# Performance work log

Measured on AMD Instinct MI355X. Metric: run time of the kernel, lower is better.

The kernel has to match this reference:

```python
import jax, jax.numpy as jnp
import numpy as np

B, X, C = 8192, 8, 512        # batch, map_num, img_dim==tex_dim
P, Y = 8, 1000                # n_prompts, cls_num
FAKE = 16                     # fake prompt width (hardcoded in module)
F = 2048                      # feat_dim
CLS = 1000                    # cls_num
IN_DIM = P * X * FAKE         # 1024
SF = 64.0


def setup_inputs() -> dict:
    key = jax.random.key(0)
    ks = jax.random.split(key, 8)
    s = 0.02
    return {
        "img_f": jax.random.normal(ks[0], (B, X, C), jnp.float32),
        "tex_f": jax.random.normal(ks[1], (P, Y, C), jnp.float32),
        "fake_cls": jax.random.normal(ks[2], (P, FAKE, C), jnp.float32),
        "fc_w": jax.random.normal(ks[3], (C, C), jnp.float32) * s,
        "fc_b": jnp.zeros((C,), jnp.float32),
        "bn1_g": jnp.ones((IN_DIM,), jnp.float32),
        "bn1_b": jnp.zeros((IN_DIM,), jnp.float32),
        "w1": jax.random.normal(ks[4], (F, IN_DIM), jnp.float32) * s,
        "b1": jnp.zeros((F,), jnp.float32),
        "bn2_g": jnp.ones((F,), jnp.float32),
        "bn2_b": jnp.zeros((F,), jnp.float32),
        "w2": jax.random.normal(ks[5], (CLS, F), jnp.float32) * s,
        "b2": jnp.zeros((CLS,), jnp.float32),
    }


def _bn(x, g, b, eps=1e-5):
    # BatchNorm1d in training mode: batch mean / biased batch var
    m = x.mean(axis=0)
    v = x.var(axis=0)
    return (x - m) * jax.lax.rsqrt(v + eps) * g + b


def reference(img_f, tex_f, fake_cls, fc_w, fc_b, bn1_g, bn1_b, w1, b1,
              bn2_g, bn2_b, w2, b2):
    # independent L2 norm over feature dim, scaled by x_sf=64
    img_n = img_f / (jnp.linalg.norm(img_f, axis=-1, keepdims=True) + 1e-6) * SF
    tex_n = tex_f / (jnp.linalg.norm(tex_f, axis=-1, keepdims=True) + 1e-6) * SF
    # prompt attention over the class axis
    tex_fc = jnp.einsum('pyc,dc->pyd', tex_n, fc_w) + fc_b          # fc(tex_f)
    attn = jax.nn.softmax(jnp.einsum('pxc,pyc->pxy', fake_cls, tex_fc), axis=-1)
    tex_a = jnp.einsum('pxy,pyc->pxc', attn, tex_n)                  # (P,16,C)
    # cross-modal relation: 'b x c, y d c -> b yxd' (icomp/tcomp are Identity)
    cp = jnp.einsum('bxc,pdc->bpxd', img_n, tex_a).reshape(img_n.shape[0], -1)
    # prt_fc: BN -> Linear -> ELU -> BN -> Linear
    h = jax.nn.elu(_bn(cp, bn1_g, bn1_b) @ w1.T + b1)
    return _bn(h, bn2_g, bn2_b) @ w2.T + b2
```

## Files before the change

kernel.cpp:

```cpp
#include <hip/hip_runtime.h>
#include <math.h>


typedef __attribute__((ext_vector_type(8))) short bf16x8;
typedef __attribute__((ext_vector_type(4))) float f32x4;

__device__ __forceinline__ float waveSum(float v) {
#pragma unroll
    for (int o = 32; o > 0; o >>= 1) v += __shfl_xor(v, o);
    return v;
}
__device__ __forceinline__ float waveMax(float v) {
#pragma unroll
    for (int o = 32; o > 0; o >>= 1) v = fmaxf(v, __shfl_xor(v, o));
    return v;
}
__device__ __forceinline__ unsigned short f2bf(float x) {
    union { float f; unsigned u; } v; v.f = x;
    unsigned r = v.u + 0x7FFFu + ((v.u >> 16) & 1u);
    return (unsigned short)(r >> 16);
}
__device__ __forceinline__ float bf2f(unsigned short h) {
    union { unsigned u; float f; } v; v.u = ((unsigned)h) << 16; return v.f;
}
__device__ __forceinline__ float bf2f_s(short h) { return bf2f((unsigned short)h); }
__device__ __forceinline__ void gload16(const void* g, const void* l) {
    __builtin_amdgcn_global_load_lds((const __attribute__((address_space(1))) void*)g,
                                     (__attribute__((address_space(3))) void*)l, 16, 0, 0);
}
__device__ __forceinline__ int xcd_swz(int d, int n) {
    int q = n >> 3;
    return (d & 7) * q + (d >> 3);
}
#define SBAR __builtin_amdgcn_sched_barrier(0)

__global__ __launch_bounds__(256) void k_prep(const float* __restrict__ tex_f,
                                              unsigned short* __restrict__ texn,
                                              const float* __restrict__ fake_cls,
                                              const float* __restrict__ fc_w,
                                              unsigned short* __restrict__ g_bf) {
    __shared__ float sred[4];
    __shared__ float fcls[512];
    int bid = blockIdx.x, t = threadIdx.x;
    if (bid < 8000) {
        const float* r = tex_f + (size_t)bid * 512;
        float2 v = *(const float2*)(r + t * 2);
        float ss = v.x * v.x + v.y * v.y;
        ss = waveSum(ss);
        if ((t & 63) == 0) sred[t >> 6] = ss;
        __syncthreads();
        float tot = sred[0] + sred[1] + sred[2] + sred[3];
        float sc = 64.f / (sqrtf(tot) + 1e-6f);
        unsigned u = (unsigned)f2bf(v.x * sc) | ((unsigned)f2bf(v.y * sc) << 16);
        *(unsigned*)(texn + (size_t)bid * 512 + t * 2) = u;
    } else {
        int row = bid - 8000;
        fcls[t]       = fake_cls[row * 512 + t];
        fcls[t + 256] = fake_cls[row * 512 + t + 256];
        __syncthreads();
        float a0 = 0.f, a1 = 0.f;
        for (int d = 0; d < 512; ++d) {
            float fv = fcls[d];
            a0 = fmaf(fv, fc_w[d * 512 + t], a0);
            a1 = fmaf(fv, fc_w[d * 512 + t + 256], a1);
        }
        g_bf[row * 512 + t]       = f2bf(a0);
        g_bf[row * 512 + t + 256] = f2bf(a1);
    }
}

__global__ __launch_bounds__(256) void k_wsum_sm(const float* __restrict__ logit,
                                                 const unsigned short* __restrict__ texn,
                                                 float* __restrict__ part) {
    int yt = blockIdx.x, p = blockIdx.y, t = threadIdx.x;
    int lane = t & 63, w = t >> 6;
    __shared__ float wl[16][63];
    __shared__ float ms[16], iss[16];
    const int y0 = yt * 63;
    const int ylen = min(63, 1000 - y0);
#pragma unroll
    for (int rr = 0; rr < 4; ++rr) {
        int x = w * 4 + rr;
        const float* lr = logit + ((size_t)p * 16 + x) * 1000;
        float m = -3.0e38f;
        for (int y = lane; y < 1000; y += 64) m = fmaxf(m, lr[y]);
        m = waveMax(m);
        float s = 0.f;
        for (int y = lane; y < 1000; y += 64) s += expf(lr[y] - m);
        s = waveSum(s);
        if (lane == 0) { ms[x] = m; iss[x] = 1.f / s; }
    }
    __syncthreads();
    for (int idx = t; idx < 16 * ylen; idx += 256) {
        int x = idx / ylen, y = idx % ylen;
        wl[x][y] = expf(logit[((size_t)p * 16 + x) * 1000 + y0 + y] - ms[x]) * iss[x];
    }
    __syncthreads();
    int c0 = t * 2;
    const unsigned short* tp = texn + ((size_t)p * 1000 + y0) * 512 + c0;
    float a0[16], a1[16];
#pragma unroll
    for (int x = 0; x < 16; ++x) { a0[x] = 0.f; a1[x] = 0.f; }
    for (int y = 0; y < ylen; ++y) {
        unsigned u = *(const unsigned*)(tp + (size_t)y * 512);
        float lo = bf2f((unsigned short)(u & 0xffff));
        float hi = bf2f((unsigned short)(u >> 16));
#pragma unroll
        for (int x = 0; x < 16; ++x) {
            float ww = wl[x][y];
            a0[x] = fmaf(ww, lo, a0[x]);
            a1[x] = fmaf(ww, hi, a1[x]);
        }
    }
#pragma unroll
    for (int x = 0; x < 16; ++x) {
        float* dst = part + ((size_t)((yt * 8 + p) * 16 + x)) * 512 + c0;
        dst[0] = a0[x];
        dst[1] = a1[x];
    }
}

__global__ __launch_bounds__(256) void k_texa_red(const float* __restrict__ part,
                                                  unsigned short* __restrict__ texa) {
    int row = blockIdx.x, t = threadIdx.x;
    int p = row >> 4, x = row & 15;
    int c = t * 2;
    float s0 = 0.f, s1 = 0.f;
#pragma unroll
    for (int yt = 0; yt < 16; ++yt) {
        const float* src = part + ((size_t)((yt * 8 + p) * 16 + x)) * 512 + c;
        s0 += src[0];
        s1 += src[1];
    }
    unsigned u = (unsigned)f2bf(s0) | ((unsigned)f2bf(s1) << 16);
    *(unsigned*)(texa + (size_t)row * 512 + c) = u;
}

__global__ __launch_bounds__(256) void k_colstat_v(const unsigned short* __restrict__ src,
                                                   float* __restrict__ ps,
                                                   float* __restrict__ pq) {
    const int cb = blockIdx.x, rb = blockIdx.y, t = threadIdx.x;
    const int tc = t & 15;
    const int tg = t >> 4;
    const unsigned short* base =
        src + (size_t)(rb * 128 + tg * 8) * 1024 + cb * 128 + tc * 8;
    float s[8], q[8];
#pragma unroll
    for (int j = 0; j < 8; ++j) { s[j] = 0.f; q[j] = 0.f; }
#pragma unroll
    for (int r = 0; r < 8; ++r) {
        bf16x8 v = *(const bf16x8*)(base + (size_t)r * 1024);
#pragma unroll
        for (int j = 0; j < 8; ++j) {
            float f = bf2f_s(v[j]);
            s[j] += f;
            q[j] = fmaf(f, f, q[j]);
        }
    }
    __shared__ float ls[16][128];
    __shared__ float lq[16][128];
#pragma unroll
    for (int j = 0; j < 8; ++j) { ls[tg][tc * 8 + j] = s[j]; lq[tg][tc * 8 + j] = q[j]; }
    __syncthreads();
    if (t < 128) {
        float S = 0.f, Q = 0.f;
#pragma unroll
        for (int g = 0; g < 16; ++g) { S += ls[g][t]; Q += lq[g][t]; }
        ps[(size_t)rb * 1024 + cb * 128 + t] = S;
        pq[(size_t)rb * 1024 + cb * 128 + t] = Q;
    }
}

template <bool PERM>
__global__ __launch_bounds__(256) void k_bnfin(const float* __restrict__ ps,
                                               const float* __restrict__ pq,
                                               const float* __restrict__ gam,
                                               const float* __restrict__ bet,
                                               float* __restrict__ a, float* __restrict__ c,
                                               int ncols) {
    int col = blockIdx.x * 256 + threadIdx.x;
    float S = 0.f, Q = 0.f;
    for (int i = 0; i < 64; ++i) {
        S += ps[(size_t)i * ncols + col];
        Q += pq[(size_t)i * ncols + col];
    }
    float mean = S * (1.f / 8192.f);
    float var = Q * (1.f / 8192.f) - mean * mean;
    int j = col;
    if (PERM) {
        int x = col >> 7, jj = col & 127, pp = jj >> 4, d = jj & 15;
        j = (pp << 7) + (x << 4) + d;
    }
    float av = gam[j] * rsqrtf(var + 1e-5f);
    a[col] = av;
    c[col] = bet[j] - mean * av;
}

template <bool PERM>
__global__ __launch_bounds__(256) void k_foldw_bf(const float* __restrict__ W,
                                                  const float* __restrict__ bin,
                                                  const float* __restrict__ a,
                                                  const float* __restrict__ c,
                                                  unsigned short* __restrict__ Wout,
                                                  float* __restrict__ bout,
                                                  int Kdim, int nvalid) {
    int f = blockIdx.x, t = threadIdx.x;
    unsigned short* wo = Wout + (size_t)f * Kdim;
    if (f >= nvalid) {
        for (int col = t; col < Kdim; col += 256) wo[col] = 0;
        if (t == 0) bout[f] = 0.f;
        return;
    }
    const float* wr = W + (size_t)f * Kdim;
    float partial = 0.f;
    for (int col = t; col < Kdim; col += 256) {
        int j = col;
        if (PERM) {
            int x = col >> 7, jj = col & 127, pp = jj >> 4, d = jj & 15;
            j = (pp << 7) + (x << 4) + d;
        }
        float wv = wr[j];
        wo[col] = f2bf(wv * a[col]);
        partial = fmaf(wv, c[col], partial);
    }
    partial = waveSum(partial);
    __shared__ float sred[4];
    if ((t & 63) == 0) sred[t >> 6] = partial;
    __syncthreads();
    if (t == 0) bout[f] = bin[f] + sred[0] + sred[1] + sred[2] + sred[3];
}

template <int EPI, bool A_F32>
__global__ __launch_bounds__(256) void gemm_mfma(const void* __restrict__ Av,
                                                 const unsigned short* __restrict__ Bv,
                                                 void* __restrict__ Cv, int K,
                                                 int ntn, int ldc, int nvalid,
                                                 int aZ, int bZ, int cZ) {
    __shared__ unsigned short Asl[128 * 64];
    __shared__ unsigned short Bsl[128 * 64];
    __shared__ float rowinv[128];
    const int tid = threadIdx.x;
    const int lane = tid & 63, wid = tid >> 6;
    const int wr = wid >> 1, wc = wid & 1;
    const int wg = xcd_swz(blockIdx.x, gridDim.x);
    const int m0 = (wg / ntn) * 128, n0 = (wg % ntn) * 128;
    const int z = blockIdx.y;

    const float* Af = (const float*)Av;
    const unsigned short* Ab = (const unsigned short*)Av + (size_t)z * aZ;
    const unsigned short* B = Bv + (size_t)z * bZ;

    f32x4 acc[4][4];
#pragma unroll
    for (int i = 0; i < 4; ++i)
#pragma unroll
        for (int j = 0; j < 4; ++j) acc[i][j] = {0.f, 0.f, 0.f, 0.f};

    const int swz = ((lane & 7) ^ (lane >> 3)) * 8;
    const int lrow = lane & 15, lkh = lane >> 4;
    float ssq[4] = {0.f, 0.f, 0.f, 0.f};

    for (int k0 = 0; k0 < K; k0 += 64) {
        if (A_F32) {
#pragma unroll
            for (int r = 0; r < 4; ++r) {
                int row = r * 32 + (tid >> 3);
                int kk = (tid & 7) * 8;
                const float* src = Af + (size_t)(m0 + row) * K + k0 + kk;
                float4 p0 = *(const float4*)src;
                float4 p1 = *(const float4*)(src + 4);
                ssq[r] += p0.x*p0.x + p0.y*p0.y + p0.z*p0.z + p0.w*p0.w
                        + p1.x*p1.x + p1.y*p1.y + p1.z*p1.z + p1.w*p1.w;
                bf16x8 v;
                v[0] = (short)f2bf(p0.x); v[1] = (short)f2bf(p0.y);
                v[2] = (short)f2bf(p0.z); v[3] = (short)f2bf(p0.w);
                v[4] = (short)f2bf(p1.x); v[5] = (short)f2bf(p1.y);
                v[6] = (short)f2bf(p1.z); v[7] = (short)f2bf(p1.w);
                *(bf16x8*)&Asl[row * 64 + (kk ^ ((row & 7) << 3))] = v;
            }
        } else {
#pragma unroll
            for (int r = 0; r < 4; ++r) {
                int row = r * 32 + wid * 8 + (lane >> 3);
                gload16(Ab + (size_t)(m0 + row) * K + k0 + swz,
                        Asl + r * 2048 + wid * 512);
            }
        }
#pragma unroll
        for (int r = 0; r < 4; ++r) {
            int row = r * 32 + wid * 8 + (lane >> 3);
            gload16(B + (size_t)(n0 + row) * K + k0 + swz,
                    Bsl + r * 2048 + wid * 512);
        }
        __syncthreads();
#pragma unroll
        for (int kk = 0; kk < 2; ++kk) {
            bf16x8 af[4], bfr[4];
#pragma unroll
            for (int m = 0; m < 4; ++m) {
                int row = wr * 64 + m * 16 + lrow;
                af[m] = *(const bf16x8*)&Asl[row * 64 + ((kk * 32 + lkh * 8) ^ ((row & 7) << 3))];
            }
#pragma unroll
            for (int n = 0; n < 4; ++n) {
                int row = wc * 64 + n * 16 + lrow;
                bfr[n] = *(const bf16x8*)&Bsl[row * 64 + ((kk * 32 + lkh * 8) ^ ((row & 7) << 3))];
            }
#pragma unroll
            for (int m = 0; m < 4; ++m)
#pragma unroll
                for (int n = 0; n < 4; ++n)
                    acc[m][n] = __builtin_amdgcn_mfma_f32_16x16x32_bf16(af[m], bfr[n], acc[m][n], 0, 0, 0);
        }
        __syncthreads();
    }

    if (A_F32) {
#pragma unroll
        for (int r = 0; r < 4; ++r) {
            float s = ssq[r];
            s += __shfl_xor(s, 1); s += __shfl_xor(s, 2); s += __shfl_xor(s, 4);
            if ((tid & 7) == 0) rowinv[r * 32 + (tid >> 3)] = 64.f / (sqrtf(s) + 1e-6f);
        }
        __syncthreads();
    }

    const int colbase = n0 + wc * 64 + lrow;
    if (EPI == 0) {
        unsigned short* C = (unsigned short*)Cv;
#pragma unroll
        for (int m = 0; m < 4; ++m) {
            int rloc = wr * 64 + m * 16 + lkh * 4;
#pragma unroll
            for (int r = 0; r < 4; ++r) {
                float riv = rowinv[rloc + r];
#pragma unroll
                for (int n = 0; n < 4; ++n)
                    C[(size_t)(m0 + rloc + r) * ldc + colbase + n * 16] = f2bf(acc[m][n][r] * riv);
            }
        }
    } else {
        float* C = (float*)Cv + (size_t)z * cZ;
#pragma unroll
        for (int m = 0; m < 4; ++m) {
            int row = m0 + wr * 64 + m * 16 + lkh * 4;
#pragma unroll
            for (int r = 0; r < 4; ++r) {
                if ((row + r) >= 16) continue;
#pragma unroll
                for (int n = 0; n < 4; ++n) {
                    int col = colbase + n * 16;
                    if (col < nvalid) C[(size_t)(row + r) * ldc + col] = acc[m][n][r];
                }
            }
        }
    }
}

template <int FM, int NH, int EPI>
__global__ __launch_bounds__(512, 2) void gemm256(const unsigned short* __restrict__ A,
                                                  const unsigned short* __restrict__ B,
                                                  void* __restrict__ Cv, int K,
                                                  int ntn, int ldc, int nvalid,
                                                  const float* __restrict__ bias,
                                                  float* __restrict__ ps,
                                                  float* __restrict__ pq) {
    constexpr int BM = FM * 32;
    constexpr int MH = BM / 128;
    constexpr int LA = 2 * (MH + NH);
    __shared__ unsigned short Asl[2][MH][128 * 64];
    __shared__ unsigned short Bsl[2][NH][128 * 64];
    const int tid = threadIdx.x;
    const int lane = tid & 63, wid = tid >> 6;
    const int wm = wid >> 2, wn = wid & 3;
    const int wg = xcd_swz(blockIdx.x, gridDim.x);
    const int m0 = (wg / ntn) * BM, n0 = (wg % ntn) * 256;
    const int lrow = lane & 15, lkh = lane >> 4;
    const int l7 = lane & 7;
    const int ksrc = ((lane & 7) ^ (lane >> 3)) * 8;
    const int mbase = wm * (BM / 2);
    const int mhalf = mbase >> 7;
    const int mloc0 = mbase & 127;
    const int nbase = wn * 64;
    const int nhalf = nbase >> 7;
    const int nloc0 = nbase & 127;

    f32x4 acc[FM][4];
#pragma unroll
    for (int m = 0; m < FM; ++m)
#pragma unroll
        for (int n = 0; n < 4; ++n) acc[m][n] = {0.f, 0.f, 0.f, 0.f};

    const int nkt = K >> 6;

    auto stage = [&](int kt, int buf) {
#pragma unroll
        for (int hf = 0; hf < MH; ++hf)
#pragma unroll
            for (int j = 0; j < 2; ++j) {
                int rl = wid * 16 + j * 8 + (lane >> 3);
                gload16(A + (size_t)(m0 + hf * 128 + rl) * K + kt * 64 + ksrc,
                        &Asl[buf][hf][(wid * 16 + j * 8) * 64]);
            }
#pragma unroll
        for (int hf = 0; hf < NH; ++hf)
#pragma unroll
            for (int j = 0; j < 2; ++j) {
                int rl = wid * 16 + j * 8 + (lane >> 3);
                gload16(B + (size_t)(n0 + hf * 128 + rl) * K + kt * 64 + ksrc,
                        &Bsl[buf][hf][(wid * 16 + j * 8) * 64]);
            }
    };

    stage(0, 0);
    stage(1, 1);
    if constexpr (LA == 8) asm volatile("s_waitcnt vmcnt(8)" ::: "memory");
    else asm volatile("s_waitcnt vmcnt(6)" ::: "memory");
    SBAR; __builtin_amdgcn_s_barrier(); SBAR;

    for (int kt = 0; kt < nkt; ++kt) {
        const int cur = kt & 1;
        bf16x8 af0[FM], bf0[4];
#pragma unroll
        for (int m = 0; m < FM; ++m) {
            int row = mloc0 + m * 16 + lrow;
            af0[m] = *(const bf16x8*)&Asl[cur][mhalf][row * 64 + ((lkh ^ l7) << 3)];
        }
#pragma unroll
        for (int n = 0; n < 4; ++n) {
            int row = nloc0 + n * 16 + lrow;
            bf0[n] = *(const bf16x8*)&Bsl[cur][nhalf][row * 64 + ((lkh ^ l7) << 3)];
        }
        __builtin_amdgcn_s_setprio(1);
#pragma unroll
        for (int m = 0; m < FM; ++m)
#pragma unroll
            for (int n = 0; n < 4; ++n)
                acc[m][n] = __builtin_amdgcn_mfma_f32_16x16x32_bf16(af0[m], bf0[n], acc[m][n], 0, 0, 0);
        __builtin_amdgcn_s_setprio(0);
        bf16x8 af1[FM], bf1[4];
#pragma unroll
        for (int m = 0; m < FM; ++m) {
            int row = mloc0 + m * 16 + lrow;
            af1[m] = *(const bf16x8*)&Asl[cur][mhalf][row * 64 + (((4 + lkh) ^ l7) << 3)];
        }
#pragma unroll
        for (int n = 0; n < 4; ++n) {
            int row = nloc0 + n * 16 + lrow;
            bf1[n] = *(const bf16x8*)&Bsl[cur][nhalf][row * 64 + (((4 + lkh) ^ l7) << 3)];
        }
        if (kt + 1 < nkt) {
            asm volatile("s_waitcnt lgkmcnt(0)" ::: "memory");
            SBAR; __builtin_amdgcn_s_barrier(); SBAR;
            if (kt + 2 < nkt) {
                stage(kt + 2, cur);
                if constexpr (LA == 8) asm volatile("s_waitcnt vmcnt(8)" ::: "memory");
                else asm volatile("s_waitcnt vmcnt(6)" ::: "memory");
            } else {
                asm volatile("s_waitcnt vmcnt(0)" ::: "memory");
            }
            SBAR; __builtin_amdgcn_s_barrier(); SBAR;
        }
        __builtin_amdgcn_s_setprio(1);
#pragma unroll
        for (int m = 0; m < FM; ++m)
#pragma unroll
            for (int n = 0; n < 4; ++n)
                acc[m][n] = __builtin_amdgcn_mfma_f32_16x16x32_bf16(af1[m], bf1[n], acc[m][n], 0, 0, 0);
        __builtin_amdgcn_s_setprio(0);
    }

    const int colbase = n0 + nbase + lrow;
    if (EPI == 1) {
        unsigned short* C = (unsigned short*)Cv;
        float bv[4], sN[4] = {0.f, 0.f, 0.f, 0.f}, qN[4] = {0.f, 0.f, 0.f, 0.f};
#pragma unroll
        for (int n = 0; n < 4; ++n) bv[n] = bias[colbase + n * 16];
#pragma unroll
        for (int m = 0; m < FM; ++m) {
            int row = m0 + mbase + m * 16 + lkh * 4;
#pragma unroll
            for (int r = 0; r < 4; ++r)
#pragma unroll
                for (int n = 0; n < 4; ++n) {
                    float v = acc[m][n][r] + bv[n];
                    v = v > 0.f ? v : expm1f(v);
                    sN[n] += v;
                    qN[n] = fmaf(v, v, qN[n]);
                    C[(size_t)(row + r) * ldc + colbase + n * 16] = f2bf(v);
                }
        }
#pragma unroll
        for (int n = 0; n < 4; ++n) {
            sN[n] += __shfl_xor(sN[n], 16); sN[n] += __shfl_xor(sN[n], 32);
            qN[n] += __shfl_xor(qN[n], 16); qN[n] += __shfl_xor(qN[n], 32);
        }
        if (lane < 16) {
            int mt = wg / ntn;
#pragma unroll
            for (int n = 0; n < 4; ++n) {
                ps[(size_t)(mt * 2 + wm) * ldc + colbase + n * 16] = sN[n];
                pq[(size_t)(mt * 2 + wm) * ldc + colbase + n * 16] = qN[n];
            }
        }
    } else {
        float* C = (float*)Cv;
        float bv[4];
#pragma unroll
        for (int n = 0; n < 4; ++n) bv[n] = bias[colbase + n * 16];
#pragma unroll
        for (int m = 0; m < FM; ++m) {
            int row = m0 + mbase + m * 16 + lkh * 4;
#pragma unroll
            for (int r = 0; r < 4; ++r)
#pragma unroll
                for (int n = 0; n < 4; ++n) {
                    int col = colbase + n * 16;
                    if (col < nvalid) C[(size_t)(row + r) * ldc + col] = acc[m][n][r] + bv[n];
                }
        }
    }
}

extern "C" void kernel_launch(void* const* d_in, const int* in_sizes, int n_in,
                              void* d_out, int out_size, void* d_ws, size_t ws_size,
                              hipStream_t stream) {
    const float* img_f    = (const float*)d_in[0];
    const float* tex_f    = (const float*)d_in[1];
    const float* fake_cls = (const float*)d_in[2];
    const float* fc_w     = (const float*)d_in[3];
    const float* bn1_g    = (const float*)d_in[5];
    const float* bn1_b    = (const float*)d_in[6];
    const float* w1       = (const float*)d_in[7];
    const float* b1       = (const float*)d_in[8];
    const float* bn2_g    = (const float*)d_in[9];
    const float* bn2_b    = (const float*)d_in[10];
    const float* w2       = (const float*)d_in[11];
    const float* b2       = (const float*)d_in[12];
    float* out = (float*)d_out;

    char* w = (char*)d_ws;
    unsigned short* texn = (unsigned short*)(w);
    unsigned short* g_bf = (unsigned short*)(w + 8388608);
    float*          logit= (float*)(w + 8650752);
    float*          part = (float*)(w + 9175040);
    unsigned short* texa = (unsigned short*)(w + 13369344);
    unsigned short* cp   = (unsigned short*)(w + 13500416);
    unsigned short* w1a  = (unsigned short*)(w + 30277632);
    float*          b1p  = (float*)(w + 34471936);
    float*          a1   = (float*)(w + 34480128);
    float*          c1   = (float*)(w + 34484224);
    float*          ps   = (float*)(w + 34488320);
    float*          pq   = (float*)(w + 35012608);
    unsigned short* h    = (unsigned short*)(w + 35536896);
    unsigned short* w2a  = (unsigned short*)(w + 69091328);
    float*          b2p  = (float*)(w + 73285632);
    float*          a2   = (float*)(w + 73289728);
    float*          c2   = (float*)(w + 73297920);

    k_prep<<<8128, 256, 0, stream>>>(tex_f, texn, fake_cls, fc_w, g_bf);
    gemm_mfma<3, false><<<dim3(8, 8), 256, 0, stream>>>(
        g_bf, texn, logit, 512, 8, 1000, 1000, 16 * 512, 1000 * 512, 16 * 1000);
    k_wsum_sm<<<dim3(16, 8), 256, 0, stream>>>(logit, texn, part);
    k_texa_red<<<128, 256, 0, stream>>>(part, texa);

    gemm_mfma<0, true><<<dim3(512, 1), 256, 0, stream>>>(
        img_f, texa, cp, 512, 1, 128, 128, 0, 0, 0);

    k_colstat_v<<<dim3(8, 64), 256, 0, stream>>>(cp, ps, pq);
    k_bnfin<true><<<4, 256, 0, stream>>>(ps, pq, bn1_g, bn1_b, a1, c1, 1024);
    k_foldw_bf<true><<<2048, 256, 0, stream>>>(w1, b1, a1, c1, w1a, b1p, 1024, 2048);

    gemm256<8, 2, 1><<<dim3(256), 512, 0, stream>>>(
        cp, w1a, h, 1024, 8, 2048, 2048, b1p, ps, pq);

    k_bnfin<false><<<8, 256, 0, stream>>>(ps, pq, bn2_g, bn2_b, a2, c2, 2048);
    k_foldw_bf<false><<<1024, 256, 0, stream>>>(w2, b2, a2, c2, w2a, b2p, 2048, 1000);

    gemm256<4, 2, 2><<<dim3(256), 512, 0, stream>>>(
        h, w2a, out, 2048, 4, 1000, 1000, b2p, nullptr, nullptr);
}
```

Before: 232.5 us.

## Fuse texa reduction via atomics and register-prefetch fp32 A tiles in cp GEMM

The k_texa_red kernel is removed. k_wsum_sm now atomically accumulates partial weighted sums straight into a zeroed fp32 texa buffer, and the cp GEMM reads that fp32 B operand and converts it to bf16 while loading it into shared memory. The fp32 img A path also prefetches the next K-slice into registers before the current tile is consumed, to hide global load latency. This saves one kernel launch and a partial-buffer round trip. In exchange it adds a memset, atomic contention, nondeterministic summation order, and extra conversion work per GEMM block on the B tile.

```diff
diff --git a/kernel.cpp b/kernel.cpp
--- a/kernel.cpp
+++ b/kernel.cpp
@@ -71,7 +71,7 @@
 
 __global__ __launch_bounds__(256) void k_wsum_sm(const float* __restrict__ logit,
                                                  const unsigned short* __restrict__ texn,
-                                                 float* __restrict__ part) {
+                                                 float* __restrict__ texa_f32) {
     int yt = blockIdx.x, p = blockIdx.y, t = threadIdx.x;
     int lane = t & 63, w = t >> 6;
     __shared__ float wl[16][63];
@@ -114,26 +114,10 @@
     }
 #pragma unroll
     for (int x = 0; x < 16; ++x) {
-        float* dst = part + ((size_t)((yt * 8 + p) * 16 + x)) * 512 + c0;
-        dst[0] = a0[x];
-        dst[1] = a1[x];
-    }
-}
-
-__global__ __launch_bounds__(256) void k_texa_red(const float* __restrict__ part,
-                                                  unsigned short* __restrict__ texa) {
-    int row = blockIdx.x, t = threadIdx.x;
-    int p = row >> 4, x = row & 15;
-    int c = t * 2;
-    float s0 = 0.f, s1 = 0.f;
-#pragma unroll
-    for (int yt = 0; yt < 16; ++yt) {
-        const float* src = part + ((size_t)((yt * 8 + p) * 16 + x)) * 512 + c;
-        s0 += src[0];
-        s1 += src[1];
-    }
-    unsigned u = (unsigned)f2bf(s0) | ((unsigned)f2bf(s1) << 16);
-    *(unsigned*)(texa + (size_t)row * 512 + c) = u;
+        float* dst = texa_f32 + (size_t)(p * 16 + x) * 512 + c0;
+        atomicAdd(dst, a0[x]);
+        atomicAdd(dst + 1, a1[x]);
+    }
 }
 
 __global__ __launch_bounds__(256) void k_colstat_v(const unsigned short* __restrict__ src,
@@ -232,7 +216,7 @@
 
 template <int EPI, bool A_F32>
 __global__ __launch_bounds__(256) void gemm_mfma(const void* __restrict__ Av,
-                                                 const unsigned short* __restrict__ Bv,
+                                                 const void* __restrict__ Bv,
                                                  void* __restrict__ Cv, int K,
                                                  int ntn, int ldc, int nvalid,
                                                  int aZ, int bZ, int cZ) {
@@ -247,8 +231,9 @@
     const int z = blockIdx.y;
 
     const float* Af = (const float*)Av;
+    const float* Bf = (const float*)Bv;
     const unsigned short* Ab = (const unsigned short*)Av + (size_t)z * aZ;
-    const unsigned short* B = Bv + (size_t)z * bZ;
+    const unsigned short* Bb = (const unsigned short*)Bv + (size_t)z * bZ;
 
     f32x4 acc[4][4];
 #pragma unroll
@@ -260,15 +245,21 @@
     const int lrow = lane & 15, lkh = lane >> 4;
     float ssq[4] = {0.f, 0.f, 0.f, 0.f};
 
-    for (int k0 = 0; k0 < K; k0 += 64) {
-        if (A_F32) {
+    if (A_F32) {
+        const int arow = tid >> 3;
+        const int akk = (tid & 7) * 8;
+        float4 a0r[4], a1r[4];
+#pragma unroll
+        for (int r = 0; r < 4; ++r) {
+            const float* s = Af + (size_t)(m0 + r * 32 + arow) * K + akk;
+            a0r[r] = *(const float4*)s;
+            a1r[r] = *(const float4*)(s + 4);
+        }
+        for (int k0 = 0; k0 < K; k0 += 64) {
 #pragma unroll
             for (int r = 0; r < 4; ++r) {
-                int row = r * 32 + (tid >> 3);
-                int kk = (tid & 7) * 8;
-                const float* src = Af + (size_t)(m0 + row) * K + k0 + kk;
-                float4 p0 = *(const float4*)src;
-                float4 p1 = *(const float4*)(src + 4);
+                int row = r * 32 + arow;
+                float4 p0 = a0r[r], p1 = a1r[r];
                 ssq[r] += p0.x*p0.x + p0.y*p0.y + p0.z*p0.z + p0.w*p0.w
                         + p1.x*p1.x + p1.y*p1.y + p1.z*p1.z + p1.w*p1.w;
                 bf16x8 v;
@@ -276,43 +267,87 @@
                 v[2] = (short)f2bf(p0.z); v[3] = (short)f2bf(p0.w);
                 v[4] = (short)f2bf(p1.x); v[5] = (short)f2bf(p1.y);
                 v[6] = (short)f2bf(p1.z); v[7] = (short)f2bf(p1.w);
-                *(bf16x8*)&Asl[row * 64 + (kk ^ ((row & 7) << 3))] = v;
-            }
-        } else {
+                *(bf16x8*)&Asl[row * 64 + (akk ^ ((row & 7) << 3))] = v;
+            }
+            if (k0 + 64 < K) {
+#pragma unroll
+                for (int r = 0; r < 4; ++r) {
+                    const float* s = Af + (size_t)(m0 + r * 32 + arow) * K + (k0 + 64) + akk;
+                    a0r[r] = *(const float4*)s;
+                    a1r[r] = *(const float4*)(s + 4);
+                }
+            }
+#pragma unroll
+            for (int r = 0; r < 4; ++r) {
+                int row = r * 32 + arow;
+                const float* s = Bf + (size_t)(n0 + row) * K + k0 + akk;
+                float4 p0 = *(const float4*)s;
+                float4 p1 = *(const float4*)(s + 4);
+                bf16x8 v;
+                v[0] = (short)f2bf(p0.x); v[1] = (short)f2bf(p0.y);
+                v[2] = (short)f2bf(p0.z); v[3] = (short)f2bf(p0.w);
+                v[4] = (short)f2bf(p1.x); v[5] = (short)f2bf(p1.y);
+                v[6] = (short)f2bf(p1.z); v[7] = (short)f2bf(p1.w);
+                *(bf16x8*)&Bsl[row * 64 + (akk ^ ((row & 7) << 3))] = v;
+            }
+            __syncthreads();
+#pragma unroll
+            for (int kk = 0; kk < 2; ++kk) {
+                bf16x8 af[4], bfr[4];
+#pragma unroll
+                for (int m = 0; m < 4; ++m) {
+                    int row = wr * 64 + m * 16 + lrow;
+                    af[m] = *(const bf16x8*)&Asl[row * 64 + ((kk * 32 + lkh * 8) ^ ((row & 7) << 3))];
+                }
+#pragma unroll
+                for (int n = 0; n < 4; ++n) {
+                    int row = wc * 64 + n * 16 + lrow;
+                    bfr[n] = *(const bf16x8*)&Bsl[row * 64 + ((kk * 32 + lkh * 8) ^ ((row & 7) << 3))];
+                }
+#pragma unroll
+                for (int m = 0; m < 4; ++m)
+#pragma unroll
+                    for (int n = 0; n < 4; ++n)
+                        acc[m][n] = __builtin_amdgcn_mfma_f32_16x16x32_bf16(af[m], bfr[n], acc[m][n], 0, 0, 0);
+            }
+            __syncthreads();
+        }
+    } else {
+        for (int k0 = 0; k0 < K; k0 += 64) {
 #pragma unroll
             for (int r = 0; r < 4; ++r) {
                 int row = r * 32 + wid * 8 + (lane >> 3);
                 gload16(Ab + (size_t)(m0 + row) * K + k0 + swz,
                         Asl + r * 2048 + wid * 512);
             }
-        }
-#pragma unroll
-        for (int r = 0; r < 4; ++r) {
-            int row = r * 32 + wid * 8 + (lane >> 3);
-            gload16(B + (size_t)(n0 + row) * K + k0 + swz,
-                    Bsl + r * 2048 + wid * 512);
-        }
-        __syncthreads();
-#pragma unroll
-        for (int kk = 0; kk < 2; ++kk) {
-            bf16x8 af[4], bfr[4];
-#pragma unroll
-            for (int m = 0; m < 4; ++m) {
-                int row = wr * 64 + m * 16 + lrow;
-                af[m] = *(const bf16x8*)&Asl[row * 64 + ((kk * 32 + lkh * 8) ^ ((row & 7) << 3))];
-            }
-#pragma unroll
-            for (int n = 0; n < 4; ++n) {
-                int row = wc * 64 + n * 16 + lrow;
-                bfr[n] = *(const bf16x8*)&Bsl[row * 64 + ((kk * 32 + lkh * 8) ^ ((row & 7) << 3))];
-            }
-#pragma unroll
-            for (int m = 0; m < 4; ++m)
-#pragma unroll
-                for (int n = 0; n < 4; ++n)
-                    acc[m][n] = __builtin_amdgcn_mfma_f32_16x16x32_bf16(af[m], bfr[n], acc[m][n], 0, 0, 0);
-        }
-        __syncthreads();
+#pragma unroll
+            for (int r = 0; r < 4; ++r) {
+                int row = r * 32 + wid * 8 + (lane >> 3);
+                gload16(Bb + (size_t)(n0 + row) * K + k0 + swz,
+                        Bsl + r * 2048 + wid * 512);
+            }
+            __syncthreads();
+#pragma unroll
+            for (int kk = 0; kk < 2; ++kk) {
+                bf16x8 af[4], bfr[4];
+#pragma unroll
+                for (int m = 0; m < 4; ++m) {
+                    int row = wr * 64 + m * 16 + lrow;
+                    af[m] = *(const bf16x8*)&Asl[row * 64 + ((kk * 32 + lkh * 8) ^ ((row & 7) << 3))];
+                }
+#pragma unroll
+                for (int n = 0; n < 4; ++n) {
+                    int row = wc * 64 + n * 16 + lrow;
+                    bfr[n] = *(const bf16x8*)&Bsl[row * 64 + ((kk * 32 + lkh * 8) ^ ((row & 7) << 3))];
+                }
+#pragma unroll
+                for (int m = 0; m < 4; ++m)
+#pragma unroll
+                    for (int n = 0; n < 4; ++n)
+                        acc[m][n] = __builtin_amdgcn_mfma_f32_16x16x32_bf16(af[m], bfr[n], acc[m][n], 0, 0, 0);
+            }
+            __syncthreads();
+        }
     }
 
     if (A_F32) {
@@ -543,8 +578,7 @@
     unsigned short* texn = (unsigned short*)(w);
     unsigned short* g_bf = (unsigned short*)(w + 8388608);
     float*          logit= (float*)(w + 8650752);
-    float*          part = (float*)(w + 9175040);
-    unsigned short* texa = (unsigned short*)(w + 13369344);
+    float*          texaf= (float*)(w + 9175040);
     unsigned short* cp   = (unsigned short*)(w + 13500416);
     unsigned short* w1a  = (unsigned short*)(w + 30277632);
     float*          b1p  = (float*)(w + 34471936);
@@ -558,14 +592,15 @@
     float*          a2   = (float*)(w + 73289728);
     float*          c2   = (float*)(w + 73297920);
 
+    hipMemsetAsync(texaf, 0, 262144, stream);
+
     k_prep<<<8128, 256, 0, stream>>>(tex_f, texn, fake_cls, fc_w, g_bf);
     gemm_mfma<3, false><<<dim3(8, 8), 256, 0, stream>>>(
         g_bf, texn, logit, 512, 8, 1000, 1000, 16 * 512, 1000 * 512, 16 * 1000);
-    k_wsum_sm<<<dim3(16, 8), 256, 0, stream>>>(logit, texn, part);
-    k_texa_red<<<128, 256, 0, stream>>>(part, texa);
+    k_wsum_sm<<<dim3(16, 8), 256, 0, stream>>>(logit, texn, texaf);
 
     gemm_mfma<0, true><<<dim3(512, 1), 256, 0, stream>>>(
-        img_f, texa, cp, 512, 1, 128, 128, 0, 0, 0);
+        img_f, texaf, cp, 512, 1, 128, 128, 0, 0, 0);
 
     k_colstat_v<<<dim3(8, 64), 256, 0, stream>>>(cp, ps, pq);
     k_bnfin<true><<<4, 256, 0, stream>>>(ps, pq, bn1_g, bn1_b, a1, c1, 1024);
```

Result: slower. 248.3 us (+6.8%).
